# Kernel tuning notes

Hardware: AMD Instinct MI355X
Metric: run time of the kernel (lower is better)

## Reference

```python
import jax, jax.numpy as jnp
import numpy as np

N_NODES = 100000
N_EDGES = 400000
N_GRAPHS = 4096
D = 300          # emb_dim
L = 5            # num_layers
NUM_ATOM, NUM_CHIR = 120, 3
NUM_BOND, NUM_DIR = 6, 3
SELF_LOOP_BOND = 4
TEMP = 0.04


def setup_inputs() -> dict:
    key = jax.random.key(0)
    ks = jax.random.split(key, 24)
    inp = {}
    # graph batch 0
    inp["x0"] = jax.random.randint(ks[0], (N_NODES, 2), 0, 3)
    inp["edge_index0"] = jax.random.randint(ks[1], (2, N_EDGES), 0, N_NODES)
    inp["edge_attr0"] = jax.random.randint(ks[2], (N_EDGES, 2), 0, 3)
    inp["batch_ids0"] = jnp.sort(jax.random.randint(ks[3], (N_NODES,), 0, N_GRAPHS))
    inp["dangling0"] = jax.random.randint(ks[4], (N_GRAPHS,), 0, N_NODES)
    # graph batch 1
    inp["x1"] = jax.random.randint(ks[5], (N_NODES, 2), 0, 3)
    inp["edge_index1"] = jax.random.randint(ks[6], (2, N_EDGES), 0, N_NODES)
    inp["edge_attr1"] = jax.random.randint(ks[7], (N_EDGES, 2), 0, 3)
    inp["batch_ids1"] = jnp.sort(jax.random.randint(ks[8], (N_NODES,), 0, N_GRAPHS))
    inp["dangling1"] = jax.random.randint(ks[9], (N_GRAPHS,), 0, N_NODES)
    # shared encoder parameters
    g = lambda i, shp, s=0.1: (jax.random.normal(ks[i], shp, jnp.float32) * s)
    inp["atom_emb1"] = g(10, (NUM_ATOM, D))
    inp["atom_emb2"] = g(11, (NUM_CHIR, D))
    inp["eemb1"] = g(12, (L, NUM_BOND, D))
    inp["eemb2"] = g(13, (L, NUM_DIR, D))
    inp["W1"] = g(14, (L, D, 2 * D))
    inp["b1"] = jnp.zeros((L, 2 * D), jnp.float32)
    inp["W2"] = g(15, (L, 2 * D, D))
    inp["b2"] = jnp.zeros((L, D), jnp.float32)
    inp["bn_g"] = jnp.ones((L, D), jnp.float32)
    inp["bn_b"] = jnp.zeros((L, D), jnp.float32)
    # projectors stacked: 0=projector0, 1=projector1, 2=dangling_proj0, 3=dangling_proj1
    inp["pW1"] = g(16, (4, D, D))
    inp["pb1"] = jnp.zeros((4, D), jnp.float32)
    inp["pW2"] = g(17, (4, D, D))
    inp["pb2"] = jnp.zeros((4, D), jnp.float32)
    return inp


def _encode(x, edge_index, edge_attr, atom_emb1, atom_emb2,
            eemb1, eemb2, W1, b1, W2, b2, bn_g, bn_b):
    # initial node embedding: sum of atom-type and chirality embeddings
    h = atom_emb1[x[:, 0]] + atom_emb2[x[:, 1]]          # [N, D]
    src, dst = edge_index[0], edge_index[1]
    for l in range(L):
        e = eemb1[l][edge_attr[:, 0]] + eemb2[l][edge_attr[:, 1]]  # [E, D]
        msg = h[src] + e                                           # [E, D]
        agg = jax.ops.segment_sum(msg, dst, num_segments=h.shape[0])
        # self-loop with bond type 4, direction 0 (pretrain-gnns GINConv)
        agg = agg + h + eemb1[l][SELF_LOOP_BOND] + eemb2[l][0]
        z = jax.nn.relu(agg @ W1[l] + b1[l]) @ W2[l] + b2[l]       # GIN MLP
        mu = jnp.mean(z, axis=0)
        var = jnp.var(z, axis=0)
        z = (z - mu) * jax.lax.rsqrt(var + 1e-5) * bn_g[l] + bn_b[l]
        h = z if l == L - 1 else jax.nn.relu(z)                    # no ReLU on last layer
    return h


def _mlp(x, w1, bb1, w2, bb2):
    return jax.nn.relu(x @ w1 + bb1) @ w2 + bb2


def _branch(h, batch_ids, dangling, proj_i, dproj_i, pW1, pb1, pW2, pb2):
    pooled = jax.ops.segment_sum(h, batch_ids, num_segments=N_GRAPHS)
    counts = jax.ops.segment_sum(jnp.ones((h.shape[0],), h.dtype), batch_ids,
                                 num_segments=N_GRAPHS)
    pooled = pooled / jnp.maximum(counts, 1.0)[:, None]            # global_mean_pool
    out = _mlp(pooled, pW1[proj_i], pb1[proj_i], pW2[proj_i], pb2[proj_i])
    out = out + _mlp(h[dangling], pW1[dproj_i], pb1[dproj_i], pW2[dproj_i], pb2[dproj_i])
    return out / jnp.linalg.norm(out, axis=1, keepdims=True)       # L2 normalize


def reference(x0, edge_index0, edge_attr0, batch_ids0, dangling0,
              x1, edge_index1, edge_attr1, batch_ids1, dangling1,
              atom_emb1, atom_emb2, eemb1, eemb2, W1, b1, W2, b2, bn_g, bn_b,
              pW1, pb1, pW2, pb2):
    h0 = _encode(x0, edge_index0, edge_attr0, atom_emb1, atom_emb2,
                 eemb1, eemb2, W1, b1, W2, b2, bn_g, bn_b)
    f0 = _branch(h0, batch_ids0, dangling0, 0, 2, pW1, pb1, pW2, pb2)
    h1 = _encode(x1, edge_index1, edge_attr1, atom_emb1, atom_emb2,
                 eemb1, eemb2, W1, b1, W2, b2, bn_g, bn_b)
    f1 = _branch(h1, batch_ids1, dangling1, 1, 3, pW1, pb1, pW2, pb2)
    logits = (f0 @ f1.T) / TEMP                                    # [G, G]
    return logits
```

## Files before the change

### kernel.cpp

```cpp
#include <hip/hip_runtime.h>

#define NN    100000
#define NE    400000
#define NG    4096
#define LL    5
#define MPAD  100096
#define NCHUNK 98

typedef unsigned short u16;
typedef __attribute__((ext_vector_type(8))) _Float16 half8;
typedef __attribute__((ext_vector_type(4))) _Float16 hv4;
typedef __attribute__((ext_vector_type(4))) float float4v;
typedef __attribute__((ext_vector_type(16))) float float16v;

__device__ __forceinline__ float b2f(u16 u){
  union { float f; unsigned u; } c; c.u = ((unsigned)u)<<16; return c.f;
}
__device__ __forceinline__ u16 f2b(float f){
  union { float f; unsigned u; } c; c.f = f;
  unsigned x = c.u;
  return (u16)((x + 0x7fffu + ((x>>16)&1u)) >> 16);
}
__device__ __forceinline__ float h2f(u16 u){
  union { u16 s; _Float16 h; } c; c.s = u; return (float)c.h;
}
__device__ __forceinline__ u16 f2h(float f){
  union { u16 s; _Float16 h; } c; c.h = (_Float16)f; return c.s;
}
__device__ __forceinline__ void g2l16(const u16* g, u16* l){
  __builtin_amdgcn_global_load_lds((const __attribute__((address_space(1))) void*)g,
                                   (__attribute__((address_space(3))) void*)l, 16, 0, 0);
}

__global__ __launch_bounds__(256) void detect_dtype(const u16* __restrict__ p, int* __restrict__ flag){
  int i = blockIdx.x*256 + threadIdx.x;
  float v = b2f(p[i]);
  if (!(fabsf(v) <= 1e4f)) atomicOr(flag, 1);
}
__global__ __launch_bounds__(256) void cvt_param(const void* __restrict__ src, u16* __restrict__ dst,
                                                 int n, const int* __restrict__ flag){
  int i = blockIdx.x*256 + threadIdx.x;
  if (i >= n) return;
  float v = (*flag) ? ((const float*)src)[i] : b2f(((const u16*)src)[i]);
  dst[i] = f2h(v);
}

__global__ __launch_bounds__(256) void zero32(unsigned* __restrict__ p, int n){
  int i = blockIdx.x*256 + threadIdx.x;
  if (i < n) p[i] = 0u;
}

__global__ __launch_bounds__(256) void tpad(const u16* __restrict__ src, u16* __restrict__ dst,
                                            int L, int K, int N, int Kp, int Np){
  int idx = blockIdx.x*256 + threadIdx.x;
  if (idx >= L*Np*Kp) return;
  int l = idx/(Np*Kp); int r = idx - l*Np*Kp; int n = r/Kp; int k = r - n*Kp;
  dst[idx] = (n<N && k<K) ? src[(l*K + k)*N + n] : (u16)0;
}

__global__ __launch_bounds__(256) void ecomb_build(const u16* __restrict__ ee1, const u16* __restrict__ ee2,
                                                   u16* __restrict__ ec){
  int idx = blockIdx.x*256 + threadIdx.x;
  if (idx >= LL*18*160) return;
  int l = idx/(18*160); int r = idx - l*18*160; int c = r/160; int p = r - c*160;
  int a0 = c/3, a1 = c - a0*3;
  u16 o0=0,o1=0;
  if (p < 150){
    int d = 2*p;
    o0 = f2h(h2f(ee1[(l*6+a0)*300+d  ]) + h2f(ee2[(l*3+a1)*300+d  ]));
    o1 = f2h(h2f(ee1[(l*6+a0)*300+d+1]) + h2f(ee2[(l*3+a1)*300+d+1]));
  }
  ((ushort2*)ec)[idx] = make_ushort2(o0,o1);
}

__global__ __launch_bounds__(256) void node_init(const int* __restrict__ x, const u16* __restrict__ ae1,
                                                 const u16* __restrict__ ae2, u16* __restrict__ h){
  int idx = blockIdx.x*256 + threadIdx.x;
  if (idx >= MPAD*160) return;
  int n = idx/160, p = idx - n*160;
  u16 o0=0,o1=0;
  if (n < NN && p < 150){
    int a = x[2*n], ch = x[2*n+1];
    int d = 2*p;
    o0 = f2h(h2f(ae1[a*300+d  ]) + h2f(ae2[ch*300+d  ]));
    o1 = f2h(h2f(ae1[a*300+d+1]) + h2f(ae2[ch*300+d+1]));
  }
  ((ushort2*)h)[idx] = make_ushort2(o0,o1);
}

__global__ __launch_bounds__(256) void hist(const int* __restrict__ ei, int* __restrict__ counts){
  int e = blockIdx.x*256 + threadIdx.x;
  if (e >= NE) return;
  atomicAdd(&counts[ei[NE + e]], 1);
}
__global__ __launch_bounds__(256) void scan_chunks(const int* __restrict__ counts, int* __restrict__ csums){
  __shared__ int sd[256];
  int base = blockIdx.x*1024;
  int s = 0;
  for (int i = threadIdx.x; i < 1024; i += 256){ int g = base+i; if (g < NN) s += counts[g]; }
  sd[threadIdx.x] = s; __syncthreads();
  for (int off=128; off>0; off>>=1){ if (threadIdx.x < off) sd[threadIdx.x] += sd[threadIdx.x+off]; __syncthreads(); }
  if (threadIdx.x == 0) csums[blockIdx.x] = sd[0];
}
__global__ __launch_bounds__(128) void scan_base(const int* __restrict__ csums, int* __restrict__ cbase,
                                                 int* __restrict__ offsets){
  __shared__ int sd[128];
  int tid = threadIdx.x;
  int v = (tid < NCHUNK) ? csums[tid] : 0;
  sd[tid] = v; __syncthreads();
  for (int off=1; off<128; off<<=1){
    int t = (tid >= off) ? sd[tid-off] : 0; __syncthreads();
    sd[tid] += t; __syncthreads();
  }
  if (tid < NCHUNK) cbase[tid] = sd[tid] - v;
  if (tid == 0) offsets[NN] = sd[NCHUNK-1];
}
__global__ __launch_bounds__(256) void scan_final(const int* __restrict__ counts, const int* __restrict__ cbase,
                                                  int* __restrict__ offsets){
  __shared__ int sd[256];
  int tid = threadIdx.x;
  int base = blockIdx.x*1024 + tid*4;
  int v0 = (base   < NN) ? counts[base  ] : 0;
  int v1 = (base+1 < NN) ? counts[base+1] : 0;
  int v2 = (base+2 < NN) ? counts[base+2] : 0;
  int v3 = (base+3 < NN) ? counts[base+3] : 0;
  int s = v0+v1+v2+v3;
  sd[tid] = s; __syncthreads();
  for (int off=1; off<256; off<<=1){
    int t = (tid >= off) ? sd[tid-off] : 0; __syncthreads();
    sd[tid] += t; __syncthreads();
  }
  int run = cbase[blockIdx.x] + sd[tid] - s;
  if (base   < NN){ offsets[base  ] = run; } run += v0;
  if (base+1 < NN){ offsets[base+1] = run; } run += v1;
  if (base+2 < NN){ offsets[base+2] = run; } run += v2;
  if (base+3 < NN){ offsets[base+3] = run; }
}
__global__ __launch_bounds__(256) void fill_perm(const int* __restrict__ ei, const int* __restrict__ ea,
                                                 const int* __restrict__ offsets,
                                                 int* __restrict__ cursor, int* __restrict__ pk){
  int e = blockIdx.x*256 + threadIdx.x;
  if (e >= NE) return;
  int d = ei[NE + e];
  int src = ei[e];
  int c = ea[2*e]*3 + ea[2*e+1];
  int pos = offsets[d] + atomicAdd(&cursor[d], 1);
  pk[pos] = src*32 + c;
}

__global__ __launch_bounds__(256) void aggregate(
    const u16* __restrict__ h, const u16* __restrict__ ecL,
    const int* __restrict__ offsets, const int* __restrict__ pk,
    u16* __restrict__ agg)
{
  __shared__ u16 ecs[18*320];
  for (int i = threadIdx.x; i < 18*160; i += 256)
    ((ushort2*)ecs)[i] = ((const ushort2*)ecL)[i];
  __syncthreads();
  int node = blockIdx.x*4 + (threadIdx.x>>6);
  int lane = threadIdx.x & 63;
  bool tl = lane < 16;
  const hv4* h4 = (const hv4*)h;
  const hv4* e4 = (const hv4*)ecs;
  long base = (long)node*80;
  hv4 acc0, acc1 = (hv4)(_Float16)0;
  acc0 = h4[base + lane] + e4[12*80 + lane];
  if (tl) acc1 = h4[base + 64 + lane] + e4[12*80 + 64 + lane];
  if (node < NN){
    int s = offsets[node], en = offsets[node+1];
    int i = s;
    while (i + 3 < en){
      int p0 = pk[i], p1 = pk[i+1], p2 = pk[i+2], p3 = pk[i+3]; i += 4;
      long b0 = (long)(p0>>5)*80, b1 = (long)(p1>>5)*80;
      long b2 = (long)(p2>>5)*80, b3 = (long)(p3>>5)*80;
      int c0 = (p0&31)*80, c1 = (p1&31)*80, c2 = (p2&31)*80, c3 = (p3&31)*80;
      hv4 a0 = h4[b0+lane], a1 = h4[b1+lane], a2 = h4[b2+lane], a3 = h4[b3+lane];
      hv4 e0 = e4[c0+lane], e1 = e4[c1+lane], e2 = e4[c2+lane], e3 = e4[c3+lane];
      acc0 += (a0+e0); acc0 += (a1+e1); acc0 += (a2+e2); acc0 += (a3+e3);
      if (tl){
        hv4 x0 = h4[b0+64+lane], x1 = h4[b1+64+lane];
        hv4 x2 = h4[b2+64+lane], x3 = h4[b3+64+lane];
        hv4 y0 = e4[c0+64+lane], y1 = e4[c1+64+lane];
        hv4 y2 = e4[c2+64+lane], y3 = e4[c3+64+lane];
        acc1 += (x0+y0); acc1 += (x1+y1); acc1 += (x2+y2); acc1 += (x3+y3);
      }
    }
    while (i < en){
      int p0 = pk[i]; ++i;
      long b0 = (long)(p0>>5)*80; int c0 = (p0&31)*80;
      acc0 += (h4[b0+lane] + e4[c0+lane]);
      if (tl) acc1 += (h4[b0+64+lane] + e4[c0+64+lane]);
    }
  }
  hv4* a4 = (hv4*)agg;
  a4[base + lane] = acc0;
  if (tl) a4[base + 64 + lane] = acc1;
}

__global__ __launch_bounds__(512, 2) void gin_mlp(
    const u16* __restrict__ A,
    const u16* __restrict__ W1Tl,
    const u16* __restrict__ b1l,
    const u16* __restrict__ W2Tl,
    const u16* __restrict__ b2l,
    u16* __restrict__ Z,
    float* __restrict__ colsum, float* __restrict__ colsumsq)
{
  __shared__ __align__(16) u16 lds[32768];
  u16* uS = lds;
  u16* Ws = lds + 8192;
  int tid = threadIdx.x;
  int wave = tid>>6, lane = tid&63;
  int n5 = lane & 31, hi = lane >> 5;
  int q = lane>>4, r = lane&15;
  int rg = wave>>1, ch = wave&1;
  int wr = wave>>2, wc = wave&3;
  int m0 = blockIdx.x*128;

  half8 aReg[20];
  const u16* Arow = A + (long)(m0 + rg*32 + n5)*320 + hi*8;
  #pragma unroll
  for (int kc=0; kc<20; ++kc) aReg[kc] = *(const half8*)(Arow + kc*16);

  float4v zacc[4][6];
  #pragma unroll
  for (int i=0;i<4;i++)
    #pragma unroll
    for (int j=0;j<6;j++) zacc[i][j] = (float4v){0.f,0.f,0.f,0.f};

  for (int t1=0; t1<10; ++t1){
    int n1_0 = t1*64;
    __syncthreads();
    #pragma unroll
    for (int rnd=0; rnd<5; ++rnd){
      int ck = rnd*512 + tid;
      int n = ck/41, k8 = ck - n*41;
      const u16* src = (k8 < 40) ? (W1Tl + (long)(n1_0 + n)*320 + k8*8) : W1Tl;
      g2l16(src, Ws + ck*8);
    }
    if (tid < 64){
      int ck = 2560 + tid;
      int n = ck/41, k8 = ck - n*41;
      const u16* src = (k8 < 40) ? (W1Tl + (long)(n1_0 + n)*320 + k8*8) : W1Tl;
      g2l16(src, Ws + ck*8);
    }
    __syncthreads();
    float16v uacc = (float16v)(0.f);
    #pragma unroll
    for (int kc=0; kc<20; ++kc){
      half8 bw = *(const half8*)&Ws[(ch*32 + n5)*328 + kc*16 + hi*8];
      uacc = __builtin_amdgcn_mfma_f32_32x32x16_f16(aReg[kc], bw, uacc, 0,0,0);
    }
    {
      int n1g = n1_0 + ch*32 + n5;
      float bv = (n1g < 600) ? h2f(b1l[n1g]) : 0.f;
      u16* uw = uS + ch*4096 + n5;
      #pragma unroll
      for (int reg=0; reg<16; ++reg){
        int row = rg*32 + (reg&3) + 8*(reg>>2) + 4*hi;
        float v = fmaxf(uacc[reg] + bv, 0.f);
        uw[row*32] = f2h(v);
      }
    }
    __syncthreads();
    #pragma unroll
    for (int i=0;i<6;i++){
      int idx = tid*8 + i*4096;
      int kc2 = idx / 12288;
      int rem = idx - kc2*12288;
      int n2 = rem >> 5, k8 = rem & 31;
      g2l16(W2Tl + (long)n2*640 + n1_0 + kc2*32 + k8, Ws + idx);
    }
    __syncthreads();
    #pragma unroll
    for (int kc2=0; kc2<2; ++kc2){
      half8 af[4], bf[6];
      #pragma unroll
      for (int i=0;i<4;i++) af[i] = *(const half8*)&uS[kc2*4096 + (wr*64+i*16+r)*32 + q*8];
      #pragma unroll
      for (int j=0;j<6;j++) bf[j] = *(const half8*)&Ws[kc2*12288 + (wc*96+j*16+r)*32 + q*8];
      #pragma unroll
      for (int i=0;i<4;i++)
        #pragma unroll
        for (int j=0;j<6;j++)
          zacc[i][j] = __builtin_amdgcn_mfma_f32_16x16x32_f16(af[i], bf[j], zacc[i][j], 0,0,0);
    }
  }
  #pragma unroll
  for (int j=0;j<6;j++){
    int c = wc*96 + j*16 + r;
    float bv = (c < 300) ? h2f(b2l[c]) : 0.f;
    float s1 = 0.f, s2 = 0.f;
    #pragma unroll
    for (int i=0;i<4;i++){
      int rowb = m0 + wr*64 + i*16 + q*4;
      #pragma unroll
      for (int t=0;t<4;t++){
        float v = zacc[i][j][t] + bv;
        int gr = rowb + t;
        if (c < 320) Z[(long)gr*320 + c] = f2h(v);
        if (gr < NN){ s1 += v; s2 += v*v; }
      }
    }
    s1 += __shfl_xor(s1,16); s1 += __shfl_xor(s1,32);
    s2 += __shfl_xor(s2,16); s2 += __shfl_xor(s2,32);
    if (q == 0 && c < 384){ atomicAdd(&colsum[c], s1); atomicAdd(&colsumsq[c], s2); }
  }
}

__global__ __launch_bounds__(256) void gemm_nt(
    const u16* __restrict__ A, int lda,
    const u16* __restrict__ BT, int ldb,
    int Kp,
    const u16* __restrict__ bias, int Nreal,
    float scale, int dorelu, int omode, int Ncap,
    void* __restrict__ Cv, int ldc,
    const int* __restrict__ outmode)
{
  __shared__ __align__(16) u16 As[128*32];
  __shared__ __align__(16) u16 Bs[128*32];
  int tid = threadIdx.x;
  int wave = tid>>6, lane = tid&63;
  int wr = (wave>>1)&1, wc = wave&1;
  int m0 = blockIdx.x*128, n0 = blockIdx.y*128;
  int q = lane>>4, r = lane&15;
  int srow = tid>>2, scol = (tid&3)*8;
  const u16* Ag0 = A  + (long)(m0+srow)*lda + scol;
  const u16* Ag1 = A  + (long)(m0+64+srow)*lda + scol;
  const u16* Bg0 = BT + (long)(n0+srow)*ldb + scol;
  const u16* Bg1 = BT + (long)(n0+64+srow)*ldb + scol;
  u16* Asl0 = &As[tid*8];
  u16* Asl1 = &As[64*32 + tid*8];
  u16* Bsl0 = &Bs[tid*8];
  u16* Bsl1 = &Bs[64*32 + tid*8];
  float4v acc[4][4];
  #pragma unroll
  for (int i=0;i<4;i++)
    #pragma unroll
    for (int j=0;j<4;j++) acc[i][j] = (float4v){0.f,0.f,0.f,0.f};

  for (int k0=0; k0<Kp; k0+=32){
    g2l16(Ag0+k0, Asl0);
    g2l16(Ag1+k0, Asl1);
    g2l16(Bg0+k0, Bsl0);
    g2l16(Bg1+k0, Bsl1);
    __syncthreads();
    half8 af[4], bf[4];
    #pragma unroll
    for (int i=0;i<4;i++) af[i] = *(const half8*)&As[(wr*64+i*16+r)*32 + q*8];
    #pragma unroll
    for (int j=0;j<4;j++) bf[j] = *(const half8*)&Bs[(wc*64+j*16+r)*32 + q*8];
    #pragma unroll
    for (int i=0;i<4;i++)
      #pragma unroll
      for (int j=0;j<4;j++)
        acc[i][j] = __builtin_amdgcn_mfma_f32_16x16x32_f16(af[i], bf[j], acc[i][j], 0,0,0);
    __syncthreads();
  }

  int ob = omode;
  if (outmode) ob = (*outmode) ? 0 : 1;
  u16* Ch = (u16*)Cv; float* Cf = (float*)Cv;
  #pragma unroll
  for (int j=0;j<4;j++){
    int c = n0 + wc*64 + j*16 + r;
    float bv = (bias && c < Nreal) ? h2f(bias[c]) : 0.f;
    #pragma unroll
    for (int i=0;i<4;i++){
      int rowb = m0 + wr*64 + i*16 + q*4;
      #pragma unroll
      for (int tt=0; tt<4; ++tt){
        float v = acc[i][j][tt] + bv;
        if (dorelu) v = fmaxf(v, 0.f);
        v *= scale;
        int gr = rowb + tt;
        if (c < Ncap){
          long o = (long)gr*ldc + c;
          if (ob == 2)      Ch[o] = f2h(v);
          else if (ob == 1) Ch[o] = f2b(v);
          else              Cf[o] = v;
        }
      }
    }
  }
}

__global__ __launch_bounds__(320) void bn_finalize(const float* __restrict__ st, const u16* __restrict__ g,
                                                   const u16* __restrict__ b, float* __restrict__ sc,
                                                   float* __restrict__ sh){
  int c = threadIdx.x;
  if (c >= 300) return;
  float mu  = st[c] * (1.0f/NN);
  float var = st[384+c] * (1.0f/NN) - mu*mu;
  float inv = rsqrtf(var + 1e-5f);
  float gg = h2f(g[c]) * inv;
  sc[c] = gg; sh[c] = h2f(b[c]) - mu*gg;
}
__global__ __launch_bounds__(256) void bn_apply(const u16* __restrict__ z, const float* __restrict__ sc,
                                                const float* __restrict__ sh, u16* __restrict__ h, int dorelu){
  int idx = blockIdx.x*256 + threadIdx.x;
  if (idx >= NN*150) return;
  int n = idx/150, p = idx - n*150;
  ushort2 zz = ((const ushort2*)z)[n*160 + p];
  int d = 2*p;
  float v0 = h2f(zz.x)*sc[d  ] + sh[d  ];
  float v1 = h2f(zz.y)*sc[d+1] + sh[d+1];
  if (dorelu){ v0 = fmaxf(v0,0.f); v1 = fmaxf(v1,0.f); }
  ((ushort2*)h)[n*160 + p] = make_ushort2(f2h(v0), f2h(v1));
}

__global__ __launch_bounds__(256) void graph_starts(const int* __restrict__ ids, int* __restrict__ starts){
  int i = blockIdx.x*256 + threadIdx.x;
  if (i >= NN) return;
  int b = ids[i];
  if (i == 0){ for (int g=0; g<=b; ++g) starts[g] = 0; }
  else { int p = ids[i-1]; for (int g=p+1; g<=b; ++g) starts[g] = i; }
  if (i == NN-1){ for (int g=b+1; g<=NG; ++g) starts[g] = NN; }
}
__global__ __launch_bounds__(256) void pool_kernel(const u16* __restrict__ h, const int* __restrict__ starts,
                                                   u16* __restrict__ pooled){
  int g = blockIdx.x*4 + (threadIdx.x>>6);
  int lane = threadIdx.x & 63;
  if (g >= NG) return;
  int s = starts[g], e = starts[g+1];
  int cnt = e - s; if (cnt < 1) cnt = 1;
  float inv = 1.0f/(float)cnt;
  float ax[3] = {0,0,0}, ay[3] = {0,0,0};
  const ushort2* h2 = (const ushort2*)h;
  for (int row=s; row<e; ++row){
    long base = (long)row*160;
    #pragma unroll
    for (int jp=0; jp<3; ++jp){
      int p = jp*64 + lane;
      if (p < 160){ ushort2 v = h2[base+p]; ax[jp] += h2f(v.x); ay[jp] += h2f(v.y); }
    }
  }
  ushort2* o2 = (ushort2*)pooled;
  #pragma unroll
  for (int jp=0; jp<3; ++jp){
    int p = jp*64 + lane;
    if (p < 160) o2[g*160+p] = make_ushort2(f2h(ax[jp]*inv), f2h(ay[jp]*inv));
  }
}
__global__ __launch_bounds__(256) void gather_rows(const u16* __restrict__ h, const int* __restrict__ idxs,
                                                   u16* __restrict__ out){
  int idx = blockIdx.x*256 + threadIdx.x;
  if (idx >= NG*160) return;
  int g = idx/160, p = idx - g*160;
  ((ushort2*)out)[idx] = ((const ushort2*)h)[(long)idxs[g]*160 + p];
}
__global__ __launch_bounds__(256) void add_norm(const float* __restrict__ vp, const float* __restrict__ vd,
                                                u16* __restrict__ f){
  int g = blockIdx.x*4 + (threadIdx.x>>6);
  int lane = threadIdx.x & 63;
  if (g >= NG) return;
  float vals[5]; float ss = 0.f;
  #pragma unroll
  for (int t=0; t<5; ++t){
    int d = lane + 64*t; float v = 0.f;
    if (d < 300) v = vp[g*320+d] + vd[g*320+d];
    vals[t] = v; ss += v*v;
  }
  #pragma unroll
  for (int off=32; off>0; off>>=1) ss += __shfl_xor(ss, off);
  float inv = rsqrtf(ss);
  #pragma unroll
  for (int t=0; t<5; ++t){
    int d = lane + 64*t;
    if (d < 320) f[g*320+d] = f2h(d < 300 ? vals[t]*inv : 0.f);
  }
}

extern "C" void kernel_launch(void* const* d_in, const int* in_sizes, int n_in,
                              void* d_out, int out_size, void* d_ws, size_t ws_size,
                              hipStream_t stream)
{
  const int* xin[2]  = {(const int*)d_in[0], (const int*)d_in[5]};
  const int* ei[2]   = {(const int*)d_in[1], (const int*)d_in[6]};
  const int* ea[2]   = {(const int*)d_in[2], (const int*)d_in[7]};
  const int* bid[2]  = {(const int*)d_in[3], (const int*)d_in[8]};
  const int* dang[2] = {(const int*)d_in[4], (const int*)d_in[9]};
  (void)in_sizes; (void)n_in; (void)out_size; (void)ws_size;

  char* w = (char*)d_ws;
  auto alloc = [&](size_t bytes)->char* {
    char* p = w; w += (bytes + 255) & ~(size_t)255; return p;
  };
  u16* hA   = (u16*)alloc((size_t)MPAD*320*2);
  u16* agg  = (u16*)alloc((size_t)MPAD*320*2);
  u16* z    = agg;
  u16*   pooled = (u16*)alloc((size_t)NG*320*2);
  u16*   hd     = (u16*)alloc((size_t)NG*320*2);
  u16*   ubuf   = (u16*)alloc((size_t)NG*384*2);
  float* vpb    = (float*)alloc((size_t)NG*320*4);
  float* vdb    = (float*)alloc((size_t)NG*320*4);
  u16* ec   = (u16*)alloc((size_t)LL*18*320*2);
  u16* W1T  = (u16*)alloc((size_t)LL*640*320*2);
  u16* W2T  = (u16*)alloc((size_t)LL*384*640*2);
  u16* pW1T = (u16*)alloc((size_t)4*384*320*2);
  u16* pW2T = (u16*)alloc((size_t)4*384*384*2);
  int* counts = (int*)alloc((size_t)NN*4);
  int* cursor = (int*)alloc((size_t)NN*4);
  int* offs   = (int*)alloc((size_t)(NN+1)*4);
  int* perm   = (int*)alloc((size_t)NE*4);
  int* csums  = (int*)alloc(512);
  int* cbase  = (int*)alloc(512);
  float* stats = (float*)alloc(768*4);
  float* bnsc  = (float*)alloc(384*4);
  float* bnsh  = (float*)alloc(384*4);
  int* starts  = (int*)alloc((size_t)(NG+1)*4);
  u16* f0b     = (u16*)alloc((size_t)NG*320*2);
  u16* f1b     = (u16*)alloc((size_t)NG*320*2);
  int* dflag   = (int*)alloc(256);
  const int pcnt[14] = {36000, 900, 9000, 4500, 900000, 3000, 900000, 1500,
                        1500, 1500, 360000, 1200, 360000, 1200};
  u16* parena = (u16*)alloc((size_t)2580300*2 + 14*256);
  u16* pp[14];
  { size_t off = 0;
    for (int i=0;i<14;i++){ pp[i] = parena + off; off += (size_t)((pcnt[i]+127)&~127); } }
  u16* ae1 = pp[0];  u16* ae2 = pp[1];  u16* ee1 = pp[2];  u16* ee2 = pp[3];
  u16* W1  = pp[4];  u16* b1  = pp[5];  u16* W2  = pp[6];  u16* b2  = pp[7];
  u16* bng = pp[8];  u16* bnb = pp[9];  u16* pW1 = pp[10]; u16* pb1 = pp[11];
  u16* pW2 = pp[12]; u16* pb2 = pp[13];

  auto cdiv = [](long a, long b){ return (int)((a + b - 1)/b); };
  auto gemm = [&](const u16* A, int lda, const u16* BT, int ldb, int Kp,
                  const u16* bias, int Nreal, float scale, int relu, int omode, int Ncap,
                  void* C, int ldc, int gx, int gy, const int* om){
    gemm_nt<<<dim3(gx,gy), 256, 0, stream>>>(A,lda,BT,ldb,Kp,bias,Nreal,scale,relu,omode,Ncap,
                                             C,ldc,om);
  };

  zero32<<<1,256,0,stream>>>((unsigned*)dflag, 1);
  detect_dtype<<<16,256,0,stream>>>((const u16*)d_in[14], dflag);
  for (int i=0;i<14;i++)
    cvt_param<<<cdiv(pcnt[i],256),256,0,stream>>>(d_in[10+i], pp[i], pcnt[i], dflag);

  tpad<<<cdiv((long)LL*640*320,256),256,0,stream>>>(W1,  W1T,  LL, 300, 600, 320, 640);
  tpad<<<cdiv((long)LL*384*640,256),256,0,stream>>>(W2,  W2T,  LL, 600, 300, 640, 384);
  tpad<<<cdiv((long)4*384*320,256),256,0,stream>>>(pW1, pW1T, 4,  300, 300, 320, 384);
  tpad<<<cdiv((long)4*384*384,256),256,0,stream>>>(pW2, pW2T, 4,  300, 300, 384, 384);
  ecomb_build<<<cdiv((long)LL*18*160,256),256,0,stream>>>(ee1, ee2, ec);

  for (int br=0; br<2; ++br){
    u16* fo = br ? f1b : f0b;
    node_init<<<cdiv((long)MPAD*160,256),256,0,stream>>>(xin[br], ae1, ae2, hA);
    zero32<<<cdiv(NN,256),256,0,stream>>>((unsigned*)counts, NN);
    hist<<<cdiv(NE,256),256,0,stream>>>(ei[br], counts);
    scan_chunks<<<NCHUNK,256,0,stream>>>(counts, csums);
    scan_base<<<1,128,0,stream>>>(csums, cbase, offs);
    scan_final<<<NCHUNK,256,0,stream>>>(counts, cbase, offs);
    zero32<<<cdiv(NN,256),256,0,stream>>>((unsigned*)cursor, NN);
    fill_perm<<<cdiv(NE,256),256,0,stream>>>(ei[br], ea[br], offs, cursor, perm);

    for (int l=0; l<LL; ++l){
      aggregate<<<MPAD/4,256,0,stream>>>(hA, ec + (size_t)l*18*320, offs, perm, agg);
      zero32<<<3,256,0,stream>>>((unsigned*)stats, 768);
      gin_mlp<<<MPAD/128, 512, 0, stream>>>(agg,
          W1T + (size_t)l*640*320, b1 + l*600,
          W2T + (size_t)l*384*640, b2 + l*300,
          z, stats, stats+384);
      bn_finalize<<<1,320,0,stream>>>(stats, bng + l*300, bnb + l*300, bnsc, bnsh);
      bn_apply<<<cdiv((long)NN*150,256),256,0,stream>>>(z, bnsc, bnsh, hA, (l < LL-1) ? 1 : 0);
    }

    graph_starts<<<cdiv(NN,256),256,0,stream>>>(bid[br], starts);
    pool_kernel<<<NG/4,256,0,stream>>>(hA, starts, pooled);
    gather_rows<<<cdiv((long)NG*160,256),256,0,stream>>>(hA, dang[br], hd);

    int pi = br, dpi = 2 + br;
    gemm(pooled, 320, pW1T + (size_t)pi*384*320, 320, 320,
         pb1 + pi*300, 300, 1.f, 1, 2, 384, ubuf, 384, NG/128, 3, nullptr);
    gemm(ubuf, 384, pW2T + (size_t)pi*384*384, 384, 384,
         pb2 + pi*300, 300, 1.f, 0, 0, 320, vpb, 320, NG/128, 3, nullptr);
    gemm(hd, 320, pW1T + (size_t)dpi*384*320, 320, 320,
         pb1 + dpi*300, 300, 1.f, 1, 2, 384, ubuf, 384, NG/128, 3, nullptr);
    gemm(ubuf, 384, pW2T + (size_t)dpi*384*384, 384, 384,
         pb2 + dpi*300, 300, 1.f, 0, 0, 320, vdb, 320, NG/128, 3, nullptr);
    add_norm<<<NG/4,256,0,stream>>>(vpb, vdb, fo);
  }

  gemm(f0b, 320, f1b, 320, 320, nullptr, 0, 25.0f, 0, 1, NG,
       d_out, NG, NG/128, NG/128, dflag);
}
```

Before: 3.695 ms.

## Double-buffer W1 tiles and prefetch W2 in gin_mlp with dynamic LDS

Restructures the gin_mlp inner loop into a software pipeline. The next W1 tile is loaded into an alternate LDS buffer and the next W2 tile is prefetched right after the current W2 GEMM, so global-to-LDS copies overlap MFMA work instead of sitting between full barriers. The first GEMM also splits its accumulation into two independent chains, and s_setprio is raised around MFMA bursts. The cost is about 146 KB of dynamic LDS per block, which likely limits the kernel to one 512-thread block per CU instead of two.

```diff
diff --git a/kernel.cpp b/kernel.cpp
--- a/kernel.cpp
+++ b/kernel.cpp
@@ -206,9 +206,11 @@
     u16* __restrict__ Z,
     float* __restrict__ colsum, float* __restrict__ colsumsq)
 {
-  __shared__ __align__(16) u16 lds[32768];
-  u16* uS = lds;
-  u16* Ws = lds + 8192;
+  extern __shared__ __align__(16) u16 lds[];
+  u16* uS   = lds;
+  u16* W1b0 = lds + 8192;
+  u16* W1b1 = lds + 8192 + 20992;
+  u16* W2s  = lds + 8192 + 2*20992;
   int tid = threadIdx.x;
   int wave = tid>>6, lane = tid&63;
   int n5 = lane & 31, hi = lane >> 5;
@@ -228,64 +230,90 @@
     #pragma unroll
     for (int j=0;j<6;j++) zacc[i][j] = (float4v){0.f,0.f,0.f,0.f};
 
-  for (int t1=0; t1<10; ++t1){
-    int n1_0 = t1*64;
-    __syncthreads();
-    #pragma unroll
-    for (int rnd=0; rnd<5; ++rnd){
-      int ck = rnd*512 + tid;
+  auto stageW1 = [&](int t, u16* dst){
+    int n1_0 = t*64;
+    #pragma unroll
+    for (int j=0;j<5;++j){
+      int ck = (wave*5 + j)*64 + lane;
       int n = ck/41, k8 = ck - n*41;
       const u16* src = (k8 < 40) ? (W1Tl + (long)(n1_0 + n)*320 + k8*8) : W1Tl;
-      g2l16(src, Ws + ck*8);
-    }
-    if (tid < 64){
-      int ck = 2560 + tid;
+      g2l16(src, dst + ck*8);
+    }
+    if (wave == 0){
+      int ck = 2560 + lane;
       int n = ck/41, k8 = ck - n*41;
       const u16* src = (k8 < 40) ? (W1Tl + (long)(n1_0 + n)*320 + k8*8) : W1Tl;
-      g2l16(src, Ws + ck*8);
-    }
-    __syncthreads();
-    float16v uacc = (float16v)(0.f);
-    #pragma unroll
-    for (int kc=0; kc<20; ++kc){
-      half8 bw = *(const half8*)&Ws[(ch*32 + n5)*328 + kc*16 + hi*8];
-      uacc = __builtin_amdgcn_mfma_f32_32x32x16_f16(aReg[kc], bw, uacc, 0,0,0);
-    }
+      g2l16(src, dst + ck*8);
+    }
+  };
+  auto stageW2 = [&](int t){
+    int n1_0 = t*64;
+    #pragma unroll
+    for (int i=0;i<6;i++){
+      int idx = tid*8 + i*4096;
+      int kc2 = idx / 12288;
+      int rem = idx - kc2*12288;
+      int n2 = rem >> 5, k8 = rem & 31;
+      g2l16(W2Tl + (long)n2*640 + n1_0 + kc2*32 + k8, W2s + idx);
+    }
+  };
+
+  stageW1(0, W1b0);
+  asm volatile("s_waitcnt vmcnt(0)" ::: "memory");
+  __builtin_amdgcn_s_barrier();
+  stageW2(0);
+
+  for (int t1=0; t1<10; ++t1){
+    const u16* Wr = (t1&1) ? W1b1 : W1b0;
+    u16* Wn       = (t1&1) ? W1b0 : W1b1;
+    if (t1 < 9) stageW1(t1+1, Wn);
+
+    float16v uacc0 = (float16v)(0.f), uacc1 = (float16v)(0.f);
+    __builtin_amdgcn_s_setprio(1);
+    #pragma unroll
+    for (int kc=0; kc<20; kc+=2){
+      half8 bw0 = *(const half8*)&Wr[(ch*32 + n5)*328 + kc*16 + hi*8];
+      half8 bw1 = *(const half8*)&Wr[(ch*32 + n5)*328 + (kc+1)*16 + hi*8];
+      uacc0 = __builtin_amdgcn_mfma_f32_32x32x16_f16(aReg[kc],   bw0, uacc0, 0,0,0);
+      uacc1 = __builtin_amdgcn_mfma_f32_32x32x16_f16(aReg[kc+1], bw1, uacc1, 0,0,0);
+    }
+    __builtin_amdgcn_s_setprio(0);
     {
-      int n1g = n1_0 + ch*32 + n5;
+      int n1g = t1*64 + ch*32 + n5;
       float bv = (n1g < 600) ? h2f(b1l[n1g]) : 0.f;
       u16* uw = uS + ch*4096 + n5;
       #pragma unroll
       for (int reg=0; reg<16; ++reg){
         int row = rg*32 + (reg&3) + 8*(reg>>2) + 4*hi;
-        float v = fmaxf(uacc[reg] + bv, 0.f);
+        float v = fmaxf(uacc0[reg] + uacc1[reg] + bv, 0.f);
         uw[row*32] = f2h(v);
       }
     }
-    __syncthreads();
-    #pragma unroll
-    for (int i=0;i<6;i++){
-      int idx = tid*8 + i*4096;
-      int kc2 = idx / 12288;
-      int rem = idx - kc2*12288;
-      int n2 = rem >> 5, k8 = rem & 31;
-      g2l16(W2Tl + (long)n2*640 + n1_0 + kc2*32 + k8, Ws + idx);
-    }
-    __syncthreads();
+    asm volatile("s_waitcnt lgkmcnt(0)" ::: "memory");
+    if (t1 == 9) asm volatile("s_waitcnt vmcnt(0)" ::: "memory");
+    else         asm volatile("s_waitcnt vmcnt(5)" ::: "memory");
+    __builtin_amdgcn_s_barrier();
+
     #pragma unroll
     for (int kc2=0; kc2<2; ++kc2){
       half8 af[4], bf[6];
       #pragma unroll
       for (int i=0;i<4;i++) af[i] = *(const half8*)&uS[kc2*4096 + (wr*64+i*16+r)*32 + q*8];
       #pragma unroll
-      for (int j=0;j<6;j++) bf[j] = *(const half8*)&Ws[kc2*12288 + (wc*96+j*16+r)*32 + q*8];
+      for (int j=0;j<6;j++) bf[j] = *(const half8*)&W2s[kc2*12288 + (wc*96+j*16+r)*32 + q*8];
+      __builtin_amdgcn_s_setprio(1);
       #pragma unroll
       for (int i=0;i<4;i++)
         #pragma unroll
         for (int j=0;j<6;j++)
           zacc[i][j] = __builtin_amdgcn_mfma_f32_16x16x32_f16(af[i], bf[j], zacc[i][j], 0,0,0);
-    }
-  }
+      __builtin_amdgcn_s_setprio(0);
+    }
+    asm volatile("s_waitcnt vmcnt(0)" ::: "memory");
+    __builtin_amdgcn_s_barrier();
+    if (t1 < 9) stageW2(t1+1);
+  }
+
   #pragma unroll
   for (int j=0;j<6;j++){
     int c = wc*96 + j*16 + r;
@@ -481,6 +509,13 @@
   const int* bid[2]  = {(const int*)d_in[3], (const int*)d_in[8]};
   const int* dang[2] = {(const int*)d_in[4], (const int*)d_in[9]};
   (void)in_sizes; (void)n_in; (void)out_size; (void)ws_size;
+
+  static bool ginAttrSet = false;
+  if (!ginAttrSet){
+    hipFuncSetAttribute(reinterpret_cast<const void*>(gin_mlp),
+                        hipFuncAttributeMaxDynamicSharedMemorySize, 149504);
+    ginAttrSet = true;
+  }
 
   char* w = (char*)d_ws;
   auto alloc = [&](size_t bytes)->char* {
@@ -556,7 +591,7 @@
     for (int l=0; l<LL; ++l){
       aggregate<<<MPAD/4,256,0,stream>>>(hA, ec + (size_t)l*18*320, offs, perm, agg);
       zero32<<<3,256,0,stream>>>((unsigned*)stats, 768);
-      gin_mlp<<<MPAD/128, 512, 0, stream>>>(agg,
+      gin_mlp<<<MPAD/128, 512, 149504, stream>>>(agg,
           W1T + (size_t)l*640*320, b1 + l*600,
           W2T + (size_t)l*384*640, b2 + l*300,
           z, stats, stats+384);
```

New measurement: 4.315 ms. 16.8% more time.

## Split fused GIN MLP into two double-buffered GEMMs with fused BN stats

Applied to the files above, without the earlier changes.

Gives the generic GEMM two LDS stages, so the next K-tile's global-to-LDS load is issued before the MFMAs on the current tile. The GEMM epilogue can now also accumulate per-column sum and sum-of-squares for batch norm. When the workspace is large enough, the fused gin_mlp kernel is replaced by two of these GEMMs, with an fp16 intermediate of width 608 written to a new large buffer. This trades the fused kernel's on-chip intermediate for extra global memory traffic in exchange for better load/compute overlap and occupancy.

```diff
diff --git a/kernel.cpp b/kernel.cpp
--- a/kernel.cpp
+++ b/kernel.cpp
@@ -315,10 +315,11 @@
     const u16* __restrict__ bias, int Nreal,
     float scale, int dorelu, int omode, int Ncap,
     void* __restrict__ Cv, int ldc,
-    const int* __restrict__ outmode)
+    const int* __restrict__ outmode,
+    float* __restrict__ cs, float* __restrict__ css)
 {
-  __shared__ __align__(16) u16 As[128*32];
-  __shared__ __align__(16) u16 Bs[128*32];
+  __shared__ __align__(16) u16 As[2][128*32];
+  __shared__ __align__(16) u16 Bs[2][128*32];
   int tid = threadIdx.x;
   int wave = tid>>6, lane = tid&63;
   int wr = (wave>>1)&1, wc = wave&1;
@@ -329,33 +330,41 @@
   const u16* Ag1 = A  + (long)(m0+64+srow)*lda + scol;
   const u16* Bg0 = BT + (long)(n0+srow)*ldb + scol;
   const u16* Bg1 = BT + (long)(n0+64+srow)*ldb + scol;
-  u16* Asl0 = &As[tid*8];
-  u16* Asl1 = &As[64*32 + tid*8];
-  u16* Bsl0 = &Bs[tid*8];
-  u16* Bsl1 = &Bs[64*32 + tid*8];
   float4v acc[4][4];
   #pragma unroll
   for (int i=0;i<4;i++)
     #pragma unroll
     for (int j=0;j<4;j++) acc[i][j] = (float4v){0.f,0.f,0.f,0.f};
 
-  for (int k0=0; k0<Kp; k0+=32){
-    g2l16(Ag0+k0, Asl0);
-    g2l16(Ag1+k0, Asl1);
-    g2l16(Bg0+k0, Bsl0);
-    g2l16(Bg1+k0, Bsl1);
-    __syncthreads();
+  g2l16(Ag0, &As[0][tid*8]);
+  g2l16(Ag1, &As[0][2048 + tid*8]);
+  g2l16(Bg0, &Bs[0][tid*8]);
+  g2l16(Bg1, &Bs[0][2048 + tid*8]);
+  asm volatile("s_waitcnt vmcnt(0)" ::: "memory");
+  __builtin_amdgcn_s_barrier();
+
+  int nk = Kp >> 5;
+  for (int t=0; t<nk; ++t){
+    int cur = t & 1, nxt = cur ^ 1;
+    if (t+1 < nk){
+      int k0 = (t+1)*32;
+      g2l16(Ag0+k0, &As[nxt][tid*8]);
+      g2l16(Ag1+k0, &As[nxt][2048 + tid*8]);
+      g2l16(Bg0+k0, &Bs[nxt][tid*8]);
+      g2l16(Bg1+k0, &Bs[nxt][2048 + tid*8]);
+    }
     half8 af[4], bf[4];
     #pragma unroll
-    for (int i=0;i<4;i++) af[i] = *(const half8*)&As[(wr*64+i*16+r)*32 + q*8];
-    #pragma unroll
-    for (int j=0;j<4;j++) bf[j] = *(const half8*)&Bs[(wc*64+j*16+r)*32 + q*8];
+    for (int i=0;i<4;i++) af[i] = *(const half8*)&As[cur][(wr*64+i*16+r)*32 + q*8];
+    #pragma unroll
+    for (int j=0;j<4;j++) bf[j] = *(const half8*)&Bs[cur][(wc*64+j*16+r)*32 + q*8];
     #pragma unroll
     for (int i=0;i<4;i++)
       #pragma unroll
       for (int j=0;j<4;j++)
         acc[i][j] = __builtin_amdgcn_mfma_f32_16x16x32_f16(af[i], bf[j], acc[i][j], 0,0,0);
-    __syncthreads();
+    asm volatile("s_waitcnt vmcnt(0)" ::: "memory");
+    __builtin_amdgcn_s_barrier();
   }
 
   int ob = omode;
@@ -365,6 +374,7 @@
   for (int j=0;j<4;j++){
     int c = n0 + wc*64 + j*16 + r;
     float bv = (bias && c < Nreal) ? h2f(bias[c]) : 0.f;
+    float s1 = 0.f, s2 = 0.f;
     #pragma unroll
     for (int i=0;i<4;i++){
       int rowb = m0 + wr*64 + i*16 + q*4;
@@ -380,7 +390,13 @@
           else if (ob == 1) Ch[o] = f2b(v);
           else              Cf[o] = v;
         }
+        if (cs && gr < NN){ s1 += v; s2 += v*v; }
       }
+    }
+    if (cs){
+      s1 += __shfl_xor(s1,16); s1 += __shfl_xor(s1,32);
+      s2 += __shfl_xor(s2,16); s2 += __shfl_xor(s2,32);
+      if (q == 0 && c < 384){ atomicAdd(&cs[c], s1); atomicAdd(&css[c], s2); }
     }
   }
 }
@@ -480,7 +496,7 @@
   const int* ea[2]   = {(const int*)d_in[2], (const int*)d_in[7]};
   const int* bid[2]  = {(const int*)d_in[3], (const int*)d_in[8]};
   const int* dang[2] = {(const int*)d_in[4], (const int*)d_in[9]};
-  (void)in_sizes; (void)n_in; (void)out_size; (void)ws_size;
+  (void)in_sizes; (void)n_in; (void)out_size;
 
   char* w = (char*)d_ws;
   auto alloc = [&](size_t bytes)->char* {
@@ -522,13 +538,16 @@
   u16* W1  = pp[4];  u16* b1  = pp[5];  u16* W2  = pp[6];  u16* b2  = pp[7];
   u16* bng = pp[8];  u16* bnb = pp[9];  u16* pW1 = pp[10]; u16* pb1 = pp[11];
   u16* pW2 = pp[12]; u16* pb2 = pp[13];
+  u16* ubig = (u16*)alloc((size_t)MPAD*608*2);
+  bool use_split = ((size_t)(w - (char*)d_ws) <= ws_size);
 
   auto cdiv = [](long a, long b){ return (int)((a + b - 1)/b); };
   auto gemm = [&](const u16* A, int lda, const u16* BT, int ldb, int Kp,
                   const u16* bias, int Nreal, float scale, int relu, int omode, int Ncap,
-                  void* C, int ldc, int gx, int gy, const int* om){
+                  void* C, int ldc, int gx, int gy, const int* om,
+                  float* cs, float* css){
     gemm_nt<<<dim3(gx,gy), 256, 0, stream>>>(A,lda,BT,ldb,Kp,bias,Nreal,scale,relu,omode,Ncap,
-                                             C,ldc,om);
+                                             C,ldc,om,cs,css);
   };
 
   zero32<<<1,256,0,stream>>>((unsigned*)dflag, 1);
@@ -556,10 +575,19 @@
     for (int l=0; l<LL; ++l){
       aggregate<<<MPAD/4,256,0,stream>>>(hA, ec + (size_t)l*18*320, offs, perm, agg);
       zero32<<<3,256,0,stream>>>((unsigned*)stats, 768);
-      gin_mlp<<<MPAD/128, 512, 0, stream>>>(agg,
-          W1T + (size_t)l*640*320, b1 + l*600,
-          W2T + (size_t)l*384*640, b2 + l*300,
-          z, stats, stats+384);
+      if (use_split){
+        gemm(agg, 320, W1T + (size_t)l*640*320, 320, 320,
+             b1 + l*600, 600, 1.f, 1, 2, 608, ubig, 608, MPAD/128, 5,
+             nullptr, nullptr, nullptr);
+        gemm(ubig, 608, W2T + (size_t)l*384*640, 640, 608,
+             b2 + l*300, 300, 1.f, 0, 2, 320, z, 320, MPAD/128, 3,
+             nullptr, stats, stats+384);
+      } else {
+        gin_mlp<<<MPAD/128, 512, 0, stream>>>(agg,
+            W1T + (size_t)l*640*320, b1 + l*600,
+            W2T + (size_t)l*384*640, b2 + l*300,
+            z, stats, stats+384);
+      }
       bn_finalize<<<1,320,0,stream>>>(stats, bng + l*300, bnb + l*300, bnsc, bnsh);
       bn_apply<<<cdiv((long)NN*150,256),256,0,stream>>>(z, bnsc, bnsh, hA, (l < LL-1) ? 1 : 0);
     }
@@ -570,16 +598,16 @@
 
     int pi = br, dpi = 2 + br;
     gemm(pooled, 320, pW1T + (size_t)pi*384*320, 320, 320,
-         pb1 + pi*300, 300, 1.f, 1, 2, 384, ubuf, 384, NG/128, 3, nullptr);
+         pb1 + pi*300, 300, 1.f, 1, 2, 384, ubuf, 384, NG/128, 3, nullptr, nullptr, nullptr);
     gemm(ubuf, 384, pW2T + (size_t)pi*384*384, 384, 384,
-         pb2 + pi*300, 300, 1.f, 0, 0, 320, vpb, 320, NG/128, 3, nullptr);
+         pb2 + pi*300, 300, 1.f, 0, 0, 320, vpb, 320, NG/128, 3, nullptr, nullptr, nullptr);
     gemm(hd, 320, pW1T + (size_t)dpi*384*320, 320, 320,
-         pb1 + dpi*300, 300, 1.f, 1, 2, 384, ubuf, 384, NG/128, 3, nullptr);
+         pb1 + dpi*300, 300, 1.f, 1, 2, 384, ubuf, 384, NG/128, 3, nullptr, nullptr, nullptr);
     gemm(ubuf, 384, pW2T + (size_t)dpi*384*384, 384, 384,
-         pb2 + dpi*300, 300, 1.f, 0, 0, 320, vdb, 320, NG/128, 3, nullptr);
+         pb2 + dpi*300, 300, 1.f, 0, 0, 320, vdb, 320, NG/128, 3, nullptr, nullptr, nullptr);
     add_norm<<<NG/4,256,0,stream>>>(vpb, vdb, fo);
   }
 
   gemm(f0b, 320, f1b, 320, 320, nullptr, 0, 25.0f, 0, 1, NG,
-       d_out, NG, NG/128, NG/128, dflag);
-}
+       d_out, NG, NG/128, NG/128, dflag, nullptr, nullptr);
+}
```

Result: no change. 3.712 ms (+0.5%).

## Replace fused GIN MLP kernel with two pipelined GEMMs over half-batches

Applied to the files above, without the earlier changes.

The fused gin_mlp kernel, which kept the hidden layer in LDS, is replaced by two calls to the generic gemm_nt kernel per half of the nodes. The intermediate 600-wide activation is written to global memory in the spare hA buffer. gemm_nt now uses a triple-buffered LDS pipeline with explicit vmcnt waits, remaps workgroups per XCD, and can accumulate batch-norm column statistics in its epilogue. bn_apply now zeros the padding columns, since hA is overwritten as scratch. This trades extra global traffic for the intermediate against better GEMM pipelining and occupancy.

```diff
diff --git a/kernel.cpp b/kernel.cpp
--- a/kernel.cpp
+++ b/kernel.cpp
@@ -5,13 +5,13 @@
 #define NG    4096
 #define LL    5
 #define MPAD  100096
+#define MHALF 50048
 #define NCHUNK 98
 
 typedef unsigned short u16;
 typedef __attribute__((ext_vector_type(8))) _Float16 half8;
 typedef __attribute__((ext_vector_type(4))) _Float16 hv4;
 typedef __attribute__((ext_vector_type(4))) float float4v;
-typedef __attribute__((ext_vector_type(16))) float float16v;
 
 __device__ __forceinline__ float b2f(u16 u){
   union { float f; unsigned u; } c; c.u = ((unsigned)u)<<16; return c.f;
@@ -197,117 +197,6 @@
   if (tl) a4[base + 64 + lane] = acc1;
 }
 
-__global__ __launch_bounds__(512, 2) void gin_mlp(
-    const u16* __restrict__ A,
-    const u16* __restrict__ W1Tl,
-    const u16* __restrict__ b1l,
-    const u16* __restrict__ W2Tl,
-    const u16* __restrict__ b2l,
-    u16* __restrict__ Z,
-    float* __restrict__ colsum, float* __restrict__ colsumsq)
-{
-  __shared__ __align__(16) u16 lds[32768];
-  u16* uS = lds;
-  u16* Ws = lds + 8192;
-  int tid = threadIdx.x;
-  int wave = tid>>6, lane = tid&63;
-  int n5 = lane & 31, hi = lane >> 5;
-  int q = lane>>4, r = lane&15;
-  int rg = wave>>1, ch = wave&1;
-  int wr = wave>>2, wc = wave&3;
-  int m0 = blockIdx.x*128;
-
-  half8 aReg[20];
-  const u16* Arow = A + (long)(m0 + rg*32 + n5)*320 + hi*8;
-  #pragma unroll
-  for (int kc=0; kc<20; ++kc) aReg[kc] = *(const half8*)(Arow + kc*16);
-
-  float4v zacc[4][6];
-  #pragma unroll
-  for (int i=0;i<4;i++)
-    #pragma unroll
-    for (int j=0;j<6;j++) zacc[i][j] = (float4v){0.f,0.f,0.f,0.f};
-
-  for (int t1=0; t1<10; ++t1){
-    int n1_0 = t1*64;
-    __syncthreads();
-    #pragma unroll
-    for (int rnd=0; rnd<5; ++rnd){
-      int ck = rnd*512 + tid;
-      int n = ck/41, k8 = ck - n*41;
-      const u16* src = (k8 < 40) ? (W1Tl + (long)(n1_0 + n)*320 + k8*8) : W1Tl;
-      g2l16(src, Ws + ck*8);
-    }
-    if (tid < 64){
-      int ck = 2560 + tid;
-      int n = ck/41, k8 = ck - n*41;
-      const u16* src = (k8 < 40) ? (W1Tl + (long)(n1_0 + n)*320 + k8*8) : W1Tl;
-      g2l16(src, Ws + ck*8);
-    }
-    __syncthreads();
-    float16v uacc = (float16v)(0.f);
-    #pragma unroll
-    for (int kc=0; kc<20; ++kc){
-      half8 bw = *(const half8*)&Ws[(ch*32 + n5)*328 + kc*16 + hi*8];
-      uacc = __builtin_amdgcn_mfma_f32_32x32x16_f16(aReg[kc], bw, uacc, 0,0,0);
-    }
-    {
-      int n1g = n1_0 + ch*32 + n5;
-      float bv = (n1g < 600) ? h2f(b1l[n1g]) : 0.f;
-      u16* uw = uS + ch*4096 + n5;
-      #pragma unroll
-      for (int reg=0; reg<16; ++reg){
-        int row = rg*32 + (reg&3) + 8*(reg>>2) + 4*hi;
-        float v = fmaxf(uacc[reg] + bv, 0.f);
-        uw[row*32] = f2h(v);
-      }
-    }
-    __syncthreads();
-    #pragma unroll
-    for (int i=0;i<6;i++){
-      int idx = tid*8 + i*4096;
-      int kc2 = idx / 12288;
-      int rem = idx - kc2*12288;
-      int n2 = rem >> 5, k8 = rem & 31;
-      g2l16(W2Tl + (long)n2*640 + n1_0 + kc2*32 + k8, Ws + idx);
-    }
-    __syncthreads();
-    #pragma unroll
-    for (int kc2=0; kc2<2; ++kc2){
-      half8 af[4], bf[6];
-      #pragma unroll
-      for (int i=0;i<4;i++) af[i] = *(const half8*)&uS[kc2*4096 + (wr*64+i*16+r)*32 + q*8];
-      #pragma unroll
-      for (int j=0;j<6;j++) bf[j] = *(const half8*)&Ws[kc2*12288 + (wc*96+j*16+r)*32 + q*8];
-      #pragma unroll
-      for (int i=0;i<4;i++)
-        #pragma unroll
-        for (int j=0;j<6;j++)
-          zacc[i][j] = __builtin_amdgcn_mfma_f32_16x16x32_f16(af[i], bf[j], zacc[i][j], 0,0,0);
-    }
-  }
-  #pragma unroll
-  for (int j=0;j<6;j++){
-    int c = wc*96 + j*16 + r;
-    float bv = (c < 300) ? h2f(b2l[c]) : 0.f;
-    float s1 = 0.f, s2 = 0.f;
-    #pragma unroll
-    for (int i=0;i<4;i++){
-      int rowb = m0 + wr*64 + i*16 + q*4;
-      #pragma unroll
-      for (int t=0;t<4;t++){
-        float v = zacc[i][j][t] + bv;
-        int gr = rowb + t;
-        if (c < 320) Z[(long)gr*320 + c] = f2h(v);
-        if (gr < NN){ s1 += v; s2 += v*v; }
-      }
-    }
-    s1 += __shfl_xor(s1,16); s1 += __shfl_xor(s1,32);
-    s2 += __shfl_xor(s2,16); s2 += __shfl_xor(s2,32);
-    if (q == 0 && c < 384){ atomicAdd(&colsum[c], s1); atomicAdd(&colsumsq[c], s2); }
-  }
-}
-
 __global__ __launch_bounds__(256) void gemm_nt(
     const u16* __restrict__ A, int lda,
     const u16* __restrict__ BT, int ldb,
@@ -315,47 +204,62 @@
     const u16* __restrict__ bias, int Nreal,
     float scale, int dorelu, int omode, int Ncap,
     void* __restrict__ Cv, int ldc,
-    const int* __restrict__ outmode)
+    const int* __restrict__ outmode,
+    float* __restrict__ cs, float* __restrict__ css, int nncap)
 {
-  __shared__ __align__(16) u16 As[128*32];
-  __shared__ __align__(16) u16 Bs[128*32];
+  __shared__ __align__(16) u16 As[3][128*32];
+  __shared__ __align__(16) u16 Bs[3][128*32];
   int tid = threadIdx.x;
   int wave = tid>>6, lane = tid&63;
   int wr = (wave>>1)&1, wc = wave&1;
-  int m0 = blockIdx.x*128, n0 = blockIdx.y*128;
+  int nwg  = gridDim.x*gridDim.y;
+  int flat = blockIdx.y*gridDim.x + blockIdx.x;
+  int qd = nwg>>3, rm = nwg&7;
+  int xcd = flat&7, sub = flat>>3;
+  int wgid = (xcd<rm ? xcd*(qd+1) : rm*(qd+1)+(xcd-rm)*qd) + sub;
+  int nt = wgid % gridDim.x, mt = wgid / gridDim.x;
+  int m0 = mt*128, n0 = nt*128;
   int q = lane>>4, r = lane&15;
   int srow = tid>>2, scol = (tid&3)*8;
   const u16* Ag0 = A  + (long)(m0+srow)*lda + scol;
   const u16* Ag1 = A  + (long)(m0+64+srow)*lda + scol;
   const u16* Bg0 = BT + (long)(n0+srow)*ldb + scol;
   const u16* Bg1 = BT + (long)(n0+64+srow)*ldb + scol;
-  u16* Asl0 = &As[tid*8];
-  u16* Asl1 = &As[64*32 + tid*8];
-  u16* Bsl0 = &Bs[tid*8];
-  u16* Bsl1 = &Bs[64*32 + tid*8];
   float4v acc[4][4];
   #pragma unroll
   for (int i=0;i<4;i++)
     #pragma unroll
     for (int j=0;j<4;j++) acc[i][j] = (float4v){0.f,0.f,0.f,0.f};
 
-  for (int k0=0; k0<Kp; k0+=32){
-    g2l16(Ag0+k0, Asl0);
-    g2l16(Ag1+k0, Asl1);
-    g2l16(Bg0+k0, Bsl0);
-    g2l16(Bg1+k0, Bsl1);
-    __syncthreads();
+  int nk = Kp >> 5;
+  {
+    g2l16(Ag0, &As[0][tid*8]);     g2l16(Ag1, &As[0][2048+tid*8]);
+    g2l16(Bg0, &Bs[0][tid*8]);     g2l16(Bg1, &Bs[0][2048+tid*8]);
+    if (nk > 1){
+      g2l16(Ag0+32, &As[1][tid*8]);  g2l16(Ag1+32, &As[1][2048+tid*8]);
+      g2l16(Bg0+32, &Bs[1][tid*8]);  g2l16(Bg1+32, &Bs[1][2048+tid*8]);
+    }
+  }
+  for (int t=0; t<nk; ++t){
+    int cur = t % 3;
+    if (t+1 < nk) asm volatile("s_waitcnt vmcnt(4)" ::: "memory");
+    else          asm volatile("s_waitcnt vmcnt(0)" ::: "memory");
+    __builtin_amdgcn_s_barrier();
+    if (t+2 < nk){
+      int b = (t+2)%3, k0 = (t+2)*32;
+      g2l16(Ag0+k0, &As[b][tid*8]);  g2l16(Ag1+k0, &As[b][2048+tid*8]);
+      g2l16(Bg0+k0, &Bs[b][tid*8]);  g2l16(Bg1+k0, &Bs[b][2048+tid*8]);
+    }
     half8 af[4], bf[4];
     #pragma unroll
-    for (int i=0;i<4;i++) af[i] = *(const half8*)&As[(wr*64+i*16+r)*32 + q*8];
+    for (int i=0;i<4;i++) af[i] = *(const half8*)&As[cur][(wr*64+i*16+r)*32 + q*8];
     #pragma unroll
-    for (int j=0;j<4;j++) bf[j] = *(const half8*)&Bs[(wc*64+j*16+r)*32 + q*8];
+    for (int j=0;j<4;j++) bf[j] = *(const half8*)&Bs[cur][(wc*64+j*16+r)*32 + q*8];
     #pragma unroll
     for (int i=0;i<4;i++)
       #pragma unroll
       for (int j=0;j<4;j++)
         acc[i][j] = __builtin_amdgcn_mfma_f32_16x16x32_f16(af[i], bf[j], acc[i][j], 0,0,0);
-    __syncthreads();
   }
 
   int ob = omode;
@@ -365,6 +269,7 @@
   for (int j=0;j<4;j++){
     int c = n0 + wc*64 + j*16 + r;
     float bv = (bias && c < Nreal) ? h2f(bias[c]) : 0.f;
+    float s1 = 0.f, s2 = 0.f;
     #pragma unroll
     for (int i=0;i<4;i++){
       int rowb = m0 + wr*64 + i*16 + q*4;
@@ -380,7 +285,13 @@
           else if (ob == 1) Ch[o] = f2b(v);
           else              Cf[o] = v;
         }
+        if (cs && gr < nncap){ s1 += v; s2 += v*v; }
       }
+    }
+    if (cs){
+      s1 += __shfl_xor(s1,16); s1 += __shfl_xor(s1,32);
+      s2 += __shfl_xor(s2,16); s2 += __shfl_xor(s2,32);
+      if (q == 0 && c < 384){ atomicAdd(&cs[c], s1); atomicAdd(&css[c], s2); }
     }
   }
 }
@@ -399,8 +310,9 @@
 __global__ __launch_bounds__(256) void bn_apply(const u16* __restrict__ z, const float* __restrict__ sc,
                                                 const float* __restrict__ sh, u16* __restrict__ h, int dorelu){
   int idx = blockIdx.x*256 + threadIdx.x;
-  if (idx >= NN*150) return;
-  int n = idx/150, p = idx - n*150;
+  if (idx >= NN*160) return;
+  int n = idx/160, p = idx - n*160;
+  if (p >= 150){ ((ushort2*)h)[n*160 + p] = make_ushort2(0,0); return; }
   ushort2 zz = ((const ushort2*)z)[n*160 + p];
   int d = 2*p;
   float v0 = h2f(zz.x)*sc[d  ] + sh[d  ];
@@ -489,6 +401,7 @@
   u16* hA   = (u16*)alloc((size_t)MPAD*320*2);
   u16* agg  = (u16*)alloc((size_t)MPAD*320*2);
   u16* z    = agg;
+  u16* ubig = hA;
   u16*   pooled = (u16*)alloc((size_t)NG*320*2);
   u16*   hd     = (u16*)alloc((size_t)NG*320*2);
   u16*   ubuf   = (u16*)alloc((size_t)NG*384*2);
@@ -526,9 +439,10 @@
   auto cdiv = [](long a, long b){ return (int)((a + b - 1)/b); };
   auto gemm = [&](const u16* A, int lda, const u16* BT, int ldb, int Kp,
                   const u16* bias, int Nreal, float scale, int relu, int omode, int Ncap,
-                  void* C, int ldc, int gx, int gy, const int* om){
+                  void* C, int ldc, int gx, int gy, const int* om,
+                  float* cs, float* css, int nncap){
     gemm_nt<<<dim3(gx,gy), 256, 0, stream>>>(A,lda,BT,ldb,Kp,bias,Nreal,scale,relu,omode,Ncap,
-                                             C,ldc,om);
+                                             C,ldc,om,cs,css,nncap);
   };
 
   zero32<<<1,256,0,stream>>>((unsigned*)dflag, 1);
@@ -556,12 +470,19 @@
     for (int l=0; l<LL; ++l){
       aggregate<<<MPAD/4,256,0,stream>>>(hA, ec + (size_t)l*18*320, offs, perm, agg);
       zero32<<<3,256,0,stream>>>((unsigned*)stats, 768);
-      gin_mlp<<<MPAD/128, 512, 0, stream>>>(agg,
-          W1T + (size_t)l*640*320, b1 + l*600,
-          W2T + (size_t)l*384*640, b2 + l*300,
-          z, stats, stats+384);
+      for (int mh=0; mh<2; ++mh){
+        const u16* Ah = agg + (size_t)mh*MHALF*320;
+        u16*       zh = z   + (size_t)mh*MHALF*320;
+        int nncap = mh ? (NN - MHALF) : MHALF;
+        gemm(Ah, 320, W1T + (size_t)l*640*320, 320, 320,
+             b1 + l*600, 600, 1.f, 1, 2, 608, ubig, 608, 5, MHALF/128,
+             nullptr, nullptr, nullptr, 0);
+        gemm(ubig, 608, W2T + (size_t)l*384*640, 640, 608,
+             b2 + l*300, 300, 1.f, 0, 2, 320, zh, 320, 3, MHALF/128,
+             nullptr, stats, stats+384, nncap);
+      }
       bn_finalize<<<1,320,0,stream>>>(stats, bng + l*300, bnb + l*300, bnsc, bnsh);
-      bn_apply<<<cdiv((long)NN*150,256),256,0,stream>>>(z, bnsc, bnsh, hA, (l < LL-1) ? 1 : 0);
+      bn_apply<<<cdiv((long)NN*160,256),256,0,stream>>>(z, bnsc, bnsh, hA, (l < LL-1) ? 1 : 0);
     }
 
     graph_starts<<<cdiv(NN,256),256,0,stream>>>(bid[br], starts);
@@ -570,16 +491,16 @@
 
     int pi = br, dpi = 2 + br;
     gemm(pooled, 320, pW1T + (size_t)pi*384*320, 320, 320,
-         pb1 + pi*300, 300, 1.f, 1, 2, 384, ubuf, 384, NG/128, 3, nullptr);
+         pb1 + pi*300, 300, 1.f, 1, 2, 384, ubuf, 384, 3, NG/128, nullptr, nullptr, nullptr, 0);
     gemm(ubuf, 384, pW2T + (size_t)pi*384*384, 384, 384,
-         pb2 + pi*300, 300, 1.f, 0, 0, 320, vpb, 320, NG/128, 3, nullptr);
+         pb2 + pi*300, 300, 1.f, 0, 0, 320, vpb, 320, 3, NG/128, nullptr, nullptr, nullptr, 0);
     gemm(hd, 320, pW1T + (size_t)dpi*384*320, 320, 320,
-         pb1 + dpi*300, 300, 1.f, 1, 2, 384, ubuf, 384, NG/128, 3, nullptr);
+         pb1 + dpi*300, 300, 1.f, 1, 2, 384, ubuf, 384, 3, NG/128, nullptr, nullptr, nullptr, 0);
     gemm(ubuf, 384, pW2T + (size_t)dpi*384*384, 384, 384,
-         pb2 + dpi*300, 300, 1.f, 0, 0, 320, vdb, 320, NG/128, 3, nullptr);
+         pb2 + dpi*300, 300, 1.f, 0, 0, 320, vdb, 320, 3, NG/128, nullptr, nullptr, nullptr, 0);
     add_norm<<<NG/4,256,0,stream>>>(vpb, vdb, fo);
   }
 
   gemm(f0b, 320, f1b, 320, 320, nullptr, 0, 25.0f, 0, 1, NG,
-       d_out, NG, NG/128, NG/128, dflag);
-}
+       d_out, NG, NG/128, NG/128, dflag, nullptr, nullptr, 0);
+}
```

Measured after the change: 4.146 ms. 1.12x slower.
